# Performance work log

Hardware: AMD Instinct MI355X
Metric: run time of the kernel (lower is better)

The kernel has to match this reference:

```python
import jax, jax.numpy as jnp
import numpy as np

B, S, T = 4, 4096, 2048
SD, TD, H = 512, 768, 8
D = SD // H
EPS = 1e-5
ALPHA_MAX = 0.5


def layer_norm(x, g, b):
    mu = jnp.mean(x, axis=-1, keepdims=True)
    var = jnp.mean(jnp.square(x - mu), axis=-1, keepdims=True)
    return (x - mu) * jax.lax.rsqrt(var + EPS) * g + b


def setup_inputs() -> dict:
    key = jax.random.key(0)
    ks = jax.random.split(key, 12)
    inp = {
        "source": jax.random.normal(ks[0], (B, S, SD), jnp.float32),
        "target": jax.random.normal(ks[1], (B, T, TD), jnp.float32),
        "target_mask": jax.random.randint(ks[2], (B, T), 0, 2, jnp.int32),
        # layer norms
        "ns_g": jnp.ones((SD,), jnp.float32), "ns_b": jnp.zeros((SD,), jnp.float32),
        "nt_g": jnp.ones((TD,), jnp.float32), "nt_b": jnp.zeros((TD,), jnp.float32),
        "no_g": jnp.ones((SD,), jnp.float32), "no_b": jnp.zeros((SD,), jnp.float32),
        # projections, stored (in, out); xavier-uniform with gains as in _init_weights
        "Wq": jax.random.uniform(ks[3], (SD, SD), jnp.float32, -1, 1) * (0.5 * np.sqrt(6.0 / (SD + SD))),
        "bq": jnp.zeros((SD,), jnp.float32),
        "Wk": jax.random.uniform(ks[4], (TD, SD), jnp.float32, -1, 1) * (0.5 * np.sqrt(6.0 / (TD + SD))),
        "bk": jnp.zeros((SD,), jnp.float32),
        "Wv": jax.random.uniform(ks[5], (TD, SD), jnp.float32, -1, 1) * (0.5 * np.sqrt(6.0 / (TD + SD))),
        "bv": jnp.zeros((SD,), jnp.float32),
        "Wo": jax.random.uniform(ks[6], (SD, SD), jnp.float32, -1, 1) * (0.25 * np.sqrt(6.0 / (SD + SD))),
        "bo": jnp.zeros((SD,), jnp.float32),
        "alpha_raw": jnp.asarray(0.1, jnp.float32),
    }
    return inp


def reference(source, target, target_mask, ns_g, ns_b, nt_g, nt_b, no_g, no_b,
              Wq, bq, Wk, bk, Wv, bv, Wo, bo, alpha_raw):
    scale = D ** -0.5
    src_n = layer_norm(source, ns_g, ns_b)
    tgt_n = layer_norm(target, nt_g, nt_b)
    Q = (src_n @ Wq + bq).reshape(B, S, H, D)
    K = (tgt_n @ Wk + bk).reshape(B, T, H, D)
    V = (tgt_n @ Wv + bv).reshape(B, T, H, D)
    attn = jnp.einsum('bshd,bthd->bhst', Q, K) * scale
    attn = jnp.clip(attn, -50.0, 50.0)
    mask = (target_mask == 0)[:, None, None, :]  # (B,1,1,T)
    attn = jnp.where(mask, -jnp.inf, attn)
    attn = jax.nn.softmax(attn, axis=-1)
    attn = jnp.nan_to_num(attn, nan=0.0)
    out = jnp.einsum('bhst,bthd->bshd', attn, V).reshape(B, S, SD)
    out = out @ Wo + bo
    out = layer_norm(out, no_g, no_b)
    alpha = ALPHA_MAX * (jnp.tanh(alpha_raw) + 1.0) / 2.0
    return source + alpha * out
```

## Files before the change

### kernel.cpp

```cpp
#include <hip/hip_runtime.h>
#include <math.h>

#define BB 4
#define SS 4096
#define TT 2048
#define SDIM 512
#define TDIM 768
#define NH 8
#define HD 64

typedef __attribute__((ext_vector_type(8))) short s8v;
typedef __attribute__((ext_vector_type(4))) short s4v;
typedef __attribute__((ext_vector_type(4))) float f32x4;
typedef __attribute__((ext_vector_type(4))) unsigned int u32x4;

__device__ inline unsigned short f2bf(float f) {
    unsigned int u = __float_as_uint(f);
    u += 0x7FFFu + ((u >> 16) & 1u);
    return (unsigned short)(u >> 16);
}

__device__ inline unsigned int cvtpk_bf16(float lo, float hi) {
    unsigned int r;
    asm("v_cvt_pk_bf16_f32 %0, %1, %2" : "=v"(r) : "v"(lo), "v"(hi));
    return r;
}

__global__ __launch_bounds__(256) void prep_w4(const float* __restrict__ W0,
                                               const float* __restrict__ W1,
                                               const float* __restrict__ W2,
                                               const float* __restrict__ W3,
                                               unsigned short* __restrict__ T0,
                                               unsigned short* __restrict__ T1,
                                               unsigned short* __restrict__ T2,
                                               unsigned short* __restrict__ T3) {
    const int z = blockIdx.z;
    const int K = (z == 1 || z == 2) ? 768 : 512;
    const int k0 = blockIdx.y * 32;
    if (k0 >= K) return;
    const float* W = (z == 0) ? W0 : (z == 1) ? W1 : (z == 2) ? W2 : W3;
    unsigned short* Wt = (z == 0) ? T0 : (z == 1) ? T1 : (z == 2) ? T2 : T3;
    const float scale = (z == 0) ? 0.125f : 1.0f;
    const int N = 512;
    __shared__ float tile[32][33];
    const int n0 = blockIdx.x * 32;
    const int tx = threadIdx.x & 31, ty = threadIdx.x >> 5;
#pragma unroll
    for (int i = 0; i < 4; ++i) {
        const int k = ty + i * 8;
        tile[k][tx] = W[(size_t)(k0 + k) * N + n0 + tx];
    }
    __syncthreads();
#pragma unroll
    for (int i = 0; i < 4; ++i) {
        const int n = ty + i * 8;
        Wt[(size_t)(n0 + n) * K + k0 + tx] = f2bf(tile[tx][n] * scale);
    }
}

template <int W, int BLK>
__global__ __launch_bounds__(BLK) void ln_rows_bf(const float* __restrict__ x,
                                                  const float* __restrict__ g,
                                                  const float* __restrict__ bb,
                                                  unsigned short* __restrict__ y) {
    const int row = blockIdx.x;
    const int t = threadIdx.x;
    float4 v = *(const float4*)(x + (size_t)row * W + t * 4);
    float s = v.x + v.y + v.z + v.w;
    float q = v.x * v.x + v.y * v.y + v.z * v.z + v.w * v.w;
#pragma unroll
    for (int off = 32; off > 0; off >>= 1) {
        s += __shfl_down(s, off, 64);
        q += __shfl_down(q, off, 64);
    }
    constexpr int NW = BLK / 64;
    __shared__ float redS[NW], redQ[NW];
    if ((t & 63) == 0) { redS[t >> 6] = s; redQ[t >> 6] = q; }
    __syncthreads();
    float S = 0.f, Q = 0.f;
#pragma unroll
    for (int i = 0; i < NW; ++i) { S += redS[i]; Q += redQ[i]; }
    const float mu = S * (1.0f / W);
    const float var = Q * (1.0f / W) - mu * mu;
    const float rstd = rsqrtf(var + 1e-5f);
    const float4 gv = *(const float4*)(g + t * 4);
    const float4 bv = *(const float4*)(bb + t * 4);
    s4v o;
    o[0] = (short)f2bf((v.x - mu) * rstd * gv.x + bv.x);
    o[1] = (short)f2bf((v.y - mu) * rstd * gv.y + bv.y);
    o[2] = (short)f2bf((v.z - mu) * rstd * gv.z + bv.z);
    o[3] = (short)f2bf((v.w - mu) * rstd * gv.w + bv.w);
    *(s4v*)(y + (size_t)row * W + t * 4) = o;
}

__global__ __launch_bounds__(128) void ln_res(const float* __restrict__ x,
                                              const float* __restrict__ src,
                                              const float* __restrict__ g,
                                              const float* __restrict__ bb,
                                              const float* __restrict__ alpha_raw,
                                              float* __restrict__ out) {
    const int W = 512;
    const int row = blockIdx.x;
    const int t = threadIdx.x;
    float4 v = *(const float4*)(x + (size_t)row * W + t * 4);
    float s = v.x + v.y + v.z + v.w;
    float q = v.x * v.x + v.y * v.y + v.z * v.z + v.w * v.w;
#pragma unroll
    for (int off = 32; off > 0; off >>= 1) {
        s += __shfl_down(s, off, 64);
        q += __shfl_down(q, off, 64);
    }
    __shared__ float redS[2], redQ[2];
    if ((t & 63) == 0) { redS[t >> 6] = s; redQ[t >> 6] = q; }
    __syncthreads();
    const float S = redS[0] + redS[1];
    const float Q = redQ[0] + redQ[1];
    const float mu = S * (1.0f / W);
    const float var = Q * (1.0f / W) - mu * mu;
    const float rstd = rsqrtf(var + 1e-5f);
    const float alpha = 0.25f * (tanhf(alpha_raw[0]) + 1.0f);
    const float4 gv = *(const float4*)(g + t * 4);
    const float4 bv = *(const float4*)(bb + t * 4);
    const float4 sv = *(const float4*)(src + (size_t)row * W + t * 4);
    float4 o;
    o.x = sv.x + alpha * ((v.x - mu) * rstd * gv.x + bv.x);
    o.y = sv.y + alpha * ((v.y - mu) * rstd * gv.y + bv.y);
    o.z = sv.z + alpha * ((v.z - mu) * rstd * gv.z + bv.z);
    o.w = sv.w + alpha * ((v.w - mu) * rstd * gv.w + bv.w);
    *(float4*)(out + (size_t)row * W + t * 4) = o;
}

template <int OUT>
__global__ __launch_bounds__(256) void gemm_mfma(const unsigned short* __restrict__ A,
                                                 const unsigned short* __restrict__ Bt,
                                                 const float* __restrict__ bias,
                                                 void* __restrict__ C,
                                                 int N, int K, float bscale) {
    __shared__ __align__(16) char A_lds[128 * 128];
    __shared__ __align__(16) char B_lds[64 * 128];
    const int tid = threadIdx.x;
    const int l = tid & 63;
    const int lq = l & 15, q = l >> 4;
    const int w = tid >> 6;
    const int wr = w >> 1, wc = w & 1;
    const int m0 = blockIdx.y * 128, n0 = blockIdx.x * 64;

    f32x4 acc[4][2];
#pragma unroll
    for (int i = 0; i < 4; ++i)
#pragma unroll
        for (int j = 0; j < 2; ++j) acc[i][j] = (f32x4){0.f, 0.f, 0.f, 0.f};

    const int sr = tid >> 1;
    const int sc = (tid & 1) * 64;
    const int swzA = (sr & 7) << 4;
    const int sr2 = tid >> 2;
    const int sc2 = (tid & 3) * 32;
    const int swzB = (sr2 & 7) << 4;

    for (int k0 = 0; k0 < K; k0 += 64) {
        const unsigned short* ap = A + (size_t)(m0 + sr) * K + k0 + (sc >> 1);
        const unsigned short* bp = Bt + (size_t)(n0 + sr2) * K + k0 + (sc2 >> 1);
#pragma unroll
        for (int c = 0; c < 4; ++c) {
            const s8v av = *(const s8v*)(ap + c * 8);
            *(s8v*)(A_lds + sr * 128 + ((sc + c * 16) ^ swzA)) = av;
        }
#pragma unroll
        for (int c = 0; c < 2; ++c) {
            const s8v bv = *(const s8v*)(bp + c * 8);
            *(s8v*)(B_lds + sr2 * 128 + ((sc2 + c * 16) ^ swzB)) = bv;
        }
        __syncthreads();
#pragma unroll
        for (int db = 0; db < 2; ++db) {
            s8v af[4], bf[2];
#pragma unroll
            for (int i = 0; i < 4; ++i) {
                const int ra = wr * 64 + i * 16 + lq;
                af[i] = *(const s8v*)(A_lds + ra * 128 + ((db * 64 + q * 16) ^ ((ra & 7) << 4)));
            }
#pragma unroll
            for (int j = 0; j < 2; ++j) {
                const int rb = wc * 32 + j * 16 + lq;
                bf[j] = *(const s8v*)(B_lds + rb * 128 + ((db * 64 + q * 16) ^ ((rb & 7) << 4)));
            }
#pragma unroll
            for (int i = 0; i < 4; ++i)
#pragma unroll
                for (int j = 0; j < 2; ++j)
                    acc[i][j] = __builtin_amdgcn_mfma_f32_16x16x32_bf16(af[i], bf[j], acc[i][j], 0, 0, 0);
        }
        __syncthreads();
    }
#pragma unroll
    for (int i = 0; i < 4; ++i) {
#pragma unroll
        for (int j = 0; j < 2; ++j) {
            const int col = n0 + wc * 32 + j * 16 + lq;
            const float bs = bias[col] * bscale;
            const int mr0 = m0 + wr * 64 + i * 16 + q * 4;
            if (OUT == 0) {
                unsigned short* Cp = (unsigned short*)C;
#pragma unroll
                for (int r = 0; r < 4; ++r)
                    Cp[(size_t)(mr0 + r) * N + col] = f2bf(acc[i][j][r] + bs);
            } else if (OUT == 1) {
                float* Cp = (float*)C;
#pragma unroll
                for (int r = 0; r < 4; ++r)
                    Cp[(size_t)(mr0 + r) * N + col] = acc[i][j][r] + bs;
            } else {
                s4v o4;
#pragma unroll
                for (int r = 0; r < 4; ++r) o4[r] = (short)f2bf(acc[i][j][r] + bs);
                unsigned short* Cp = (unsigned short*)C;
                *(s4v*)(Cp + ((size_t)((mr0 >> 11) * SDIM + col)) * TT + (mr0 & 2047)) = o4;
            }
        }
    }
}

__global__ __launch_bounds__(256) void attn_mfma(const unsigned short* __restrict__ Qg,
                                                 const unsigned short* __restrict__ Kg,
                                                 const unsigned short* __restrict__ Vt,
                                                 const int* __restrict__ mask,
                                                 unsigned short* __restrict__ O) {
    __shared__ __align__(16) char K_lds[2][64 * 128];
    __shared__ __align__(16) char V_lds[2][64 * 128];
    __shared__ __align__(16) float Msb[2][64];
    const int b = blockIdx.y >> 3, h = blockIdx.y & 7;
    const int tid = threadIdx.x;
    const int w = tid >> 6, l = tid & 63;
    const int lq = l & 15, q = l >> 4;
    const int qbase = blockIdx.x * 128 + w * 32;

    s8v qf[2][2];
#pragma unroll
    for (int qa = 0; qa < 2; ++qa) {
        const unsigned short* qp = Qg + ((size_t)b * SS + qbase + qa * 16 + lq) * SDIM + h * HD + q * 8;
        qf[qa][0] = *(const s8v*)(qp);
        qf[qa][1] = *(const s8v*)(qp + 32);
    }
    f32x4 accO[2][4];
#pragma unroll
    for (int qa = 0; qa < 2; ++qa)
#pragma unroll
        for (int nt = 0; nt < 4; ++nt) accO[qa][nt] = (f32x4){0.f, 0.f, 0.f, 0.f};
    float lsum[2] = {0.f, 0.f};

    const int sr = tid >> 2;
    const int scb = (tid & 3) * 32;
    const int swz = (sr & 7) << 4;
    const unsigned short* kp_base = Kg + ((size_t)b * TT + sr) * SDIM + h * HD + (scb >> 1);
    const unsigned short* vp_base = Vt + ((size_t)(b * SDIM + h * HD + sr)) * TT + (scb >> 1);

    {
        const s8v k0r = *(const s8v*)kp_base;
        const s8v k1r = *(const s8v*)(kp_base + 8);
        const s8v v0r = *(const s8v*)vp_base;
        const s8v v1r = *(const s8v*)(vp_base + 8);
        *(s8v*)(K_lds[0] + sr * 128 + (scb ^ swz)) = k0r;
        *(s8v*)(K_lds[0] + sr * 128 + ((scb + 16) ^ swz)) = k1r;
        *(s8v*)(V_lds[0] + sr * 128 + (scb ^ swz)) = v0r;
        *(s8v*)(V_lds[0] + sr * 128 + ((scb + 16) ^ swz)) = v1r;
        if (tid < 64) Msb[0][tid] = (mask[b * TT + tid] == 0) ? -1e30f : 0.f;
    }
    __syncthreads();

    for (int t0 = 0; t0 < TT; t0 += 64) {
        const int cur = (t0 >> 6) & 1, nxt = cur ^ 1;
        const bool has_next = (t0 + 64) < TT;

        s8v kn0, kn1, vn0, vn1;
        int mn = 0;
        if (has_next) {
            const unsigned short* kp = kp_base + (size_t)(t0 + 64) * SDIM;
            const unsigned short* vp = vp_base + (t0 + 64);
            kn0 = *(const s8v*)kp;
            kn1 = *(const s8v*)(kp + 8);
            vn0 = *(const s8v*)vp;
            vn1 = *(const s8v*)(vp + 8);
            if (tid < 64) mn = mask[b * TT + t0 + 64 + tid];
        }

        u32x4 pb[2][2];
#pragma unroll
        for (int kt = 0; kt < 4; ++kt) {
            const int row = kt * 16 + lq;
            const int rs = (row & 7) << 4;
            const f32x4 mb = *(const f32x4*)(&Msb[cur][kt * 16 + q * 4]);
            f32x4 aS0 = mb, aS1 = mb;
            __builtin_amdgcn_s_setprio(1);
#pragma unroll
            for (int db = 0; db < 2; ++db) {
                const s8v af = *(const s8v*)(K_lds[cur] + row * 128 + ((db * 64 + q * 16) ^ rs));
                aS0 = __builtin_amdgcn_mfma_f32_16x16x32_bf16(af, qf[0][db], aS0, 0, 0, 0);
                aS1 = __builtin_amdgcn_mfma_f32_16x16x32_bf16(af, qf[1][db], aS1, 0, 0, 0);
            }
            __builtin_amdgcn_s_setprio(0);
            {
                const float p0 = __expf(aS0[0]), p1 = __expf(aS0[1]);
                const float p2 = __expf(aS0[2]), p3 = __expf(aS0[3]);
                lsum[0] += (p0 + p1) + (p2 + p3);
                pb[kt >> 1][0][(kt & 1) * 2 + 0] = cvtpk_bf16(p0, p1);
                pb[kt >> 1][0][(kt & 1) * 2 + 1] = cvtpk_bf16(p2, p3);
            }
            {
                const float p0 = __expf(aS1[0]), p1 = __expf(aS1[1]);
                const float p2 = __expf(aS1[2]), p3 = __expf(aS1[3]);
                lsum[1] += (p0 + p1) + (p2 + p3);
                pb[kt >> 1][1][(kt & 1) * 2 + 0] = cvtpk_bf16(p0, p1);
                pb[kt >> 1][1][(kt & 1) * 2 + 1] = cvtpk_bf16(p2, p3);
            }
        }
#pragma unroll
        for (int kb = 0; kb < 2; ++kb) {
            const s8v pb0 = __builtin_bit_cast(s8v, pb[kb][0]);
            const s8v pb1 = __builtin_bit_cast(s8v, pb[kb][1]);
            __builtin_amdgcn_s_setprio(1);
#pragma unroll
            for (int nt = 0; nt < 4; ++nt) {
                const int row = nt * 16 + lq;
                const int rs = (row & 7) << 4;
                const s4v lo = *(const s4v*)(V_lds[cur] + row * 128 + ((kb * 64 + q * 8) ^ rs));
                const s4v hi = *(const s4v*)(V_lds[cur] + row * 128 + ((kb * 64 + 32 + q * 8) ^ rs));
                const s8v vf = __builtin_shufflevector(lo, hi, 0, 1, 2, 3, 4, 5, 6, 7);
                accO[0][nt] = __builtin_amdgcn_mfma_f32_16x16x32_bf16(vf, pb0, accO[0][nt], 0, 0, 0);
                accO[1][nt] = __builtin_amdgcn_mfma_f32_16x16x32_bf16(vf, pb1, accO[1][nt], 0, 0, 0);
            }
            __builtin_amdgcn_s_setprio(0);
        }

        if (has_next) {
            *(s8v*)(K_lds[nxt] + sr * 128 + (scb ^ swz)) = kn0;
            *(s8v*)(K_lds[nxt] + sr * 128 + ((scb + 16) ^ swz)) = kn1;
            *(s8v*)(V_lds[nxt] + sr * 128 + (scb ^ swz)) = vn0;
            *(s8v*)(V_lds[nxt] + sr * 128 + ((scb + 16) ^ swz)) = vn1;
            if (tid < 64) Msb[nxt][tid] = (mn == 0) ? -1e30f : 0.f;
        }
        __syncthreads();
    }

#pragma unroll
    for (int qa = 0; qa < 2; ++qa) {
        float ls = lsum[qa];
        ls += __shfl_xor(ls, 16, 64);
        ls += __shfl_xor(ls, 32, 64);
        const float inv = (ls > 0.f) ? 1.0f / ls : 0.f;
        unsigned short* op = O + ((size_t)b * SS + qbase + qa * 16 + lq) * SDIM + h * HD + q * 4;
#pragma unroll
        for (int nt = 0; nt < 4; ++nt) {
            s4v o4;
#pragma unroll
            for (int r = 0; r < 4; ++r) o4[r] = (short)f2bf(accO[qa][nt][r] * inv);
            *(s4v*)(op + nt * 16) = o4;
        }
    }
}

extern "C" void kernel_launch(void* const* d_in, const int* in_sizes, int n_in,
                              void* d_out, int out_size, void* d_ws, size_t ws_size,
                              hipStream_t stream) {
    const float* src = (const float*)d_in[0];
    const float* tgt = (const float*)d_in[1];
    const int* tmask = (const int*)d_in[2];
    const float* ns_g = (const float*)d_in[3];
    const float* ns_b = (const float*)d_in[4];
    const float* nt_g = (const float*)d_in[5];
    const float* nt_b = (const float*)d_in[6];
    const float* no_g = (const float*)d_in[7];
    const float* no_b = (const float*)d_in[8];
    const float* Wq = (const float*)d_in[9];
    const float* bq = (const float*)d_in[10];
    const float* Wk = (const float*)d_in[11];
    const float* bk = (const float*)d_in[12];
    const float* Wv = (const float*)d_in[13];
    const float* bv = (const float*)d_in[14];
    const float* Wo = (const float*)d_in[15];
    const float* bo = (const float*)d_in[16];
    const float* alpha_raw = (const float*)d_in[17];

    char* ws = (char*)d_ws;
    unsigned short* src_n = (unsigned short*)ws; ws += (size_t)16384 * 512 * 2;
    unsigned short* tgt_n = (unsigned short*)ws; ws += (size_t)8192 * 768 * 2;
    unsigned short* Qb    = (unsigned short*)ws; ws += (size_t)16384 * 512 * 2;
    unsigned short* Kb    = (unsigned short*)ws; ws += (size_t)8192 * 512 * 2;
    unsigned short* Vtb   = (unsigned short*)ws; ws += (size_t)8192 * 512 * 2;
    unsigned short* Oa    = (unsigned short*)ws; ws += (size_t)16384 * 512 * 2;
    float*          Opj   = (float*)ws;          ws += (size_t)16384 * 512 * 4;
    unsigned short* Wtq   = (unsigned short*)ws; ws += (size_t)512 * 512 * 2;
    unsigned short* Wtk   = (unsigned short*)ws; ws += (size_t)512 * 768 * 2;
    unsigned short* Wtv   = (unsigned short*)ws; ws += (size_t)512 * 768 * 2;
    unsigned short* Wto   = (unsigned short*)ws; ws += (size_t)512 * 512 * 2;

    prep_w4<<<dim3(16, 24, 4), 256, 0, stream>>>(Wq, Wk, Wv, Wo, Wtq, Wtk, Wtv, Wto);

    ln_rows_bf<512, 128><<<16384, 128, 0, stream>>>(src, ns_g, ns_b, src_n);
    ln_rows_bf<768, 192><<<8192, 192, 0, stream>>>(tgt, nt_g, nt_b, tgt_n);

    gemm_mfma<0><<<dim3(8, 128), 256, 0, stream>>>(src_n, Wtq, bq, Qb, 512, 512, 0.125f);
    gemm_mfma<0><<<dim3(8, 64), 256, 0, stream>>>(tgt_n, Wtk, bk, Kb, 512, 768, 1.0f);
    gemm_mfma<2><<<dim3(8, 64), 256, 0, stream>>>(tgt_n, Wtv, bv, Vtb, 512, 768, 1.0f);

    attn_mfma<<<dim3(32, 32), 256, 0, stream>>>(Qb, Kb, Vtb, tmask, Oa);

    gemm_mfma<1><<<dim3(8, 128), 256, 0, stream>>>(Oa, Wto, bo, Opj, 512, 512, 1.0f);

    ln_res<<<16384, 128, 0, stream>>>(Opj, src, no_g, no_b, alpha_raw, (float*)d_out);
}
```

Baseline: 349.5 us.

## Use direct global-to-LDS loads in GEMM and attention, enlarge GEMM tile

Replaces register-staged global loads followed by LDS stores with global_load_lds (16-byte direct-to-LDS) in both the projection GEMM and the attention K/V pipeline. The swizzle moves to the global source address so the LDS layout matches the existing reads. The GEMM tile also grows from 128x64 to 128x128, which halves the grid and gives each wave a 4x4 MFMA block, and adds setprio around the MFMA burst. The aims are fewer VGPRs and VALU instructions per load and more reuse per tile. The trade-off is fewer GEMM blocks and a correctness dependence on how the async LDS writes are ordered against the barriers.

```diff
diff --git a/kernel.cpp b/kernel.cpp
--- a/kernel.cpp
+++ b/kernel.cpp
@@ -24,6 +24,10 @@
     unsigned int r;
     asm("v_cvt_pk_bf16_f32 %0, %1, %2" : "=v"(r) : "v"(lo), "v"(hi));
     return r;
+}
+
+__device__ inline void glds16(const void* g, void* l) {
+    __builtin_amdgcn_global_load_lds((const unsigned int*)g, (unsigned int*)l, 16, 0, 0);
 }
 
 __global__ __launch_bounds__(256) void prep_w4(const float* __restrict__ W0,
@@ -137,67 +141,62 @@
                                                  void* __restrict__ C,
                                                  int N, int K, float bscale) {
     __shared__ __align__(16) char A_lds[128 * 128];
-    __shared__ __align__(16) char B_lds[64 * 128];
+    __shared__ __align__(16) char B_lds[128 * 128];
     const int tid = threadIdx.x;
-    const int l = tid & 63;
+    const int l = tid & 63, w = tid >> 6;
     const int lq = l & 15, q = l >> 4;
-    const int w = tid >> 6;
     const int wr = w >> 1, wc = w & 1;
-    const int m0 = blockIdx.y * 128, n0 = blockIdx.x * 64;
-
-    f32x4 acc[4][2];
+    const int m0 = blockIdx.y * 128, n0 = blockIdx.x * 128;
+
+    const int rsub = l >> 3;
+    const int colb = ((l & 7) ^ rsub) << 4;
+    const char* aSrc[4];
+    const char* bSrc[4];
+#pragma unroll
+    for (int i = 0; i < 4; ++i) {
+        const int row = (w * 4 + i) * 8 + rsub;
+        aSrc[i] = (const char*)A + (size_t)(m0 + row) * K * 2 + colb;
+        bSrc[i] = (const char*)Bt + (size_t)(n0 + row) * K * 2 + colb;
+    }
+
+    f32x4 acc[4][4];
 #pragma unroll
     for (int i = 0; i < 4; ++i)
 #pragma unroll
-        for (int j = 0; j < 2; ++j) acc[i][j] = (f32x4){0.f, 0.f, 0.f, 0.f};
-
-    const int sr = tid >> 1;
-    const int sc = (tid & 1) * 64;
-    const int swzA = (sr & 7) << 4;
-    const int sr2 = tid >> 2;
-    const int sc2 = (tid & 3) * 32;
-    const int swzB = (sr2 & 7) << 4;
+        for (int j = 0; j < 4; ++j) acc[i][j] = (f32x4){0.f, 0.f, 0.f, 0.f};
 
     for (int k0 = 0; k0 < K; k0 += 64) {
-        const unsigned short* ap = A + (size_t)(m0 + sr) * K + k0 + (sc >> 1);
-        const unsigned short* bp = Bt + (size_t)(n0 + sr2) * K + k0 + (sc2 >> 1);
-#pragma unroll
-        for (int c = 0; c < 4; ++c) {
-            const s8v av = *(const s8v*)(ap + c * 8);
-            *(s8v*)(A_lds + sr * 128 + ((sc + c * 16) ^ swzA)) = av;
-        }
-#pragma unroll
-        for (int c = 0; c < 2; ++c) {
-            const s8v bv = *(const s8v*)(bp + c * 8);
-            *(s8v*)(B_lds + sr2 * 128 + ((sc2 + c * 16) ^ swzB)) = bv;
-        }
         __syncthreads();
 #pragma unroll
+        for (int i = 0; i < 4; ++i) {
+            glds16(aSrc[i] + (size_t)k0 * 2, A_lds + (w * 4 + i) * 1024);
+            glds16(bSrc[i] + (size_t)k0 * 2, B_lds + (w * 4 + i) * 1024);
+        }
+        __syncthreads();
+#pragma unroll
         for (int db = 0; db < 2; ++db) {
-            s8v af[4], bf[2];
+            s8v af[4], bf[4];
 #pragma unroll
             for (int i = 0; i < 4; ++i) {
                 const int ra = wr * 64 + i * 16 + lq;
                 af[i] = *(const s8v*)(A_lds + ra * 128 + ((db * 64 + q * 16) ^ ((ra & 7) << 4)));
-            }
-#pragma unroll
-            for (int j = 0; j < 2; ++j) {
-                const int rb = wc * 32 + j * 16 + lq;
-                bf[j] = *(const s8v*)(B_lds + rb * 128 + ((db * 64 + q * 16) ^ ((rb & 7) << 4)));
-            }
+                const int rb = wc * 64 + i * 16 + lq;
+                bf[i] = *(const s8v*)(B_lds + rb * 128 + ((db * 64 + q * 16) ^ ((rb & 7) << 4)));
+            }
+            __builtin_amdgcn_s_setprio(1);
 #pragma unroll
             for (int i = 0; i < 4; ++i)
 #pragma unroll
-                for (int j = 0; j < 2; ++j)
+                for (int j = 0; j < 4; ++j)
                     acc[i][j] = __builtin_amdgcn_mfma_f32_16x16x32_bf16(af[i], bf[j], acc[i][j], 0, 0, 0);
-        }
-        __syncthreads();
+            __builtin_amdgcn_s_setprio(0);
+        }
     }
 #pragma unroll
     for (int i = 0; i < 4; ++i) {
 #pragma unroll
-        for (int j = 0; j < 2; ++j) {
-            const int col = n0 + wc * 32 + j * 16 + lq;
+        for (int j = 0; j < 4; ++j) {
+            const int col = n0 + wc * 64 + j * 16 + lq;
             const float bs = bias[col] * bscale;
             const int mr0 = m0 + wr * 64 + i * 16 + q * 4;
             if (OUT == 0) {
@@ -249,38 +248,36 @@
         for (int nt = 0; nt < 4; ++nt) accO[qa][nt] = (f32x4){0.f, 0.f, 0.f, 0.f};
     float lsum[2] = {0.f, 0.f};
 
-    const int sr = tid >> 2;
-    const int scb = (tid & 3) * 32;
-    const int swz = (sr & 7) << 4;
-    const unsigned short* kp_base = Kg + ((size_t)b * TT + sr) * SDIM + h * HD + (scb >> 1);
-    const unsigned short* vp_base = Vt + ((size_t)(b * SDIM + h * HD + sr)) * TT + (scb >> 1);
-
-    {
-        const s8v k0r = *(const s8v*)kp_base;
-        const s8v k1r = *(const s8v*)(kp_base + 8);
-        const s8v v0r = *(const s8v*)vp_base;
-        const s8v v1r = *(const s8v*)(vp_base + 8);
-        *(s8v*)(K_lds[0] + sr * 128 + (scb ^ swz)) = k0r;
-        *(s8v*)(K_lds[0] + sr * 128 + ((scb + 16) ^ swz)) = k1r;
-        *(s8v*)(V_lds[0] + sr * 128 + (scb ^ swz)) = v0r;
-        *(s8v*)(V_lds[0] + sr * 128 + ((scb + 16) ^ swz)) = v1r;
-        if (tid < 64) Msb[0][tid] = (mask[b * TT + tid] == 0) ? -1e30f : 0.f;
-    }
+    const int rsub = l >> 3;
+    const int colb = ((l & 7) ^ rsub) << 4;
+    const char* kSrc[2];
+    const char* vSrc[2];
+#pragma unroll
+    for (int i = 0; i < 2; ++i) {
+        const int row = (w * 2 + i) * 8 + rsub;
+        kSrc[i] = (const char*)Kg + ((size_t)(b * TT + row) * SDIM + h * HD) * 2 + colb;
+        vSrc[i] = (const char*)Vt + ((size_t)(b * SDIM + h * HD + row)) * TT * 2 + colb;
+    }
+
+#pragma unroll
+    for (int i = 0; i < 2; ++i) {
+        glds16(kSrc[i], K_lds[0] + (w * 2 + i) * 1024);
+        glds16(vSrc[i], V_lds[0] + (w * 2 + i) * 1024);
+    }
+    if (tid < 64) Msb[0][tid] = (mask[b * TT + tid] == 0) ? -1e30f : 0.f;
     __syncthreads();
 
     for (int t0 = 0; t0 < TT; t0 += 64) {
         const int cur = (t0 >> 6) & 1, nxt = cur ^ 1;
         const bool has_next = (t0 + 64) < TT;
 
-        s8v kn0, kn1, vn0, vn1;
         int mn = 0;
         if (has_next) {
-            const unsigned short* kp = kp_base + (size_t)(t0 + 64) * SDIM;
-            const unsigned short* vp = vp_base + (t0 + 64);
-            kn0 = *(const s8v*)kp;
-            kn1 = *(const s8v*)(kp + 8);
-            vn0 = *(const s8v*)vp;
-            vn1 = *(const s8v*)(vp + 8);
+#pragma unroll
+            for (int i = 0; i < 2; ++i) {
+                glds16(kSrc[i] + (size_t)(t0 + 64) * SDIM * 2, K_lds[nxt] + (w * 2 + i) * 1024);
+                glds16(vSrc[i] + (size_t)(t0 + 64) * 2, V_lds[nxt] + (w * 2 + i) * 1024);
+            }
             if (tid < 64) mn = mask[b * TT + t0 + 64 + tid];
         }
 
@@ -332,13 +329,7 @@
             __builtin_amdgcn_s_setprio(0);
         }
 
-        if (has_next) {
-            *(s8v*)(K_lds[nxt] + sr * 128 + (scb ^ swz)) = kn0;
-            *(s8v*)(K_lds[nxt] + sr * 128 + ((scb + 16) ^ swz)) = kn1;
-            *(s8v*)(V_lds[nxt] + sr * 128 + (scb ^ swz)) = vn0;
-            *(s8v*)(V_lds[nxt] + sr * 128 + ((scb + 16) ^ swz)) = vn1;
-            if (tid < 64) Msb[nxt][tid] = (mn == 0) ? -1e30f : 0.f;
-        }
+        if (has_next && tid < 64) Msb[nxt][tid] = (mn == 0) ? -1e30f : 0.f;
         __syncthreads();
     }
 
@@ -399,13 +390,13 @@
     ln_rows_bf<512, 128><<<16384, 128, 0, stream>>>(src, ns_g, ns_b, src_n);
     ln_rows_bf<768, 192><<<8192, 192, 0, stream>>>(tgt, nt_g, nt_b, tgt_n);
 
-    gemm_mfma<0><<<dim3(8, 128), 256, 0, stream>>>(src_n, Wtq, bq, Qb, 512, 512, 0.125f);
-    gemm_mfma<0><<<dim3(8, 64), 256, 0, stream>>>(tgt_n, Wtk, bk, Kb, 512, 768, 1.0f);
-    gemm_mfma<2><<<dim3(8, 64), 256, 0, stream>>>(tgt_n, Wtv, bv, Vtb, 512, 768, 1.0f);
+    gemm_mfma<0><<<dim3(4, 128), 256, 0, stream>>>(src_n, Wtq, bq, Qb, 512, 512, 0.125f);
+    gemm_mfma<0><<<dim3(4, 64), 256, 0, stream>>>(tgt_n, Wtk, bk, Kb, 512, 768, 1.0f);
+    gemm_mfma<2><<<dim3(4, 64), 256, 0, stream>>>(tgt_n, Wtv, bv, Vtb, 512, 768, 1.0f);
 
     attn_mfma<<<dim3(32, 32), 256, 0, stream>>>(Qb, Kb, Vtb, tmask, Oa);
 
-    gemm_mfma<1><<<dim3(8, 128), 256, 0, stream>>>(Oa, Wto, bo, Opj, 512, 512, 1.0f);
+    gemm_mfma<1><<<dim3(4, 128), 256, 0, stream>>>(Oa, Wto, bo, Opj, 512, 512, 1.0f);
 
     ln_res<<<16384, 128, 0, stream>>>(Opj, src, no_g, no_b, alpha_raw, (float*)d_out);
 }
```

Result: faster. 328.0 us (-6.1%).
